# Kernel optimization log

Hardware: AMD Instinct MI355X
Metric: run time of the kernel (lower is better)

The kernel has to match this reference:

```python
import jax, jax.numpy as jnp
import numpy as np

N, IN, OUT = 8192, 4096, 4096
EPS = 1e-5


def setup_inputs() -> dict:
    key = jax.random.key(0)
    k1, k2, k3, k4, k5 = jax.random.split(key, 5)
    return {
        "input": jax.random.normal(k1, (N, IN), dtype=jnp.float32),
        "weight": jax.random.randint(k2, (OUT, IN // 8), 0, 256, dtype=jnp.int32),
        "weight_scale": jax.random.uniform(k3, (OUT,), dtype=jnp.float32, minval=0.5, maxval=1.5),
        "input_factor": jax.random.uniform(k4, (IN,), dtype=jnp.float32, minval=0.5, maxval=1.5),
        "bias": jax.random.normal(k5, (OUT,), dtype=jnp.float32) * 0.01,
    }


def _unpack_pm1(weight_packed, dtype):
    # weight_packed: [OUT, IN//8] packed bytes; bit b of byte j -> column j*8+b
    shifts = jnp.arange(8, dtype=weight_packed.dtype)  # [8]
    bits = (weight_packed[:, :, None] >> shifts) & 1   # [OUT, IN//8, 8]
    w = (1 - 2 * bits).astype(dtype)                   # bit 0 -> +1, bit 1 -> -1
    return w.reshape(weight_packed.shape[0], -1)        # [OUT, IN]


def reference(input, weight, weight_scale, input_factor, bias):
    x = input * input_factor[None, :]                   # [N, IN]
    w = _unpack_pm1(weight, x.dtype)                    # [OUT, IN]
    out = jnp.einsum("ni,oi->no", x, w)                # [N, OUT]
    out = out * weight_scale[None, :]
    # LayerNorm over OUT, no affine
    mean = jnp.mean(out, axis=-1, keepdims=True)
    var = jnp.var(out, axis=-1, keepdims=True)
    out = (out - mean) * jax.lax.rsqrt(var + EPS)
    return out + bias[None, :]
```

## Files before the change

### kernel.cpp

```cpp
#include <hip/hip_runtime.h>
#include <hip/hip_bf16.h>
#include <stdint.h>

#define N_ROWS 8192
#define IN_DIM 4096
#define OUT_DIM 4096
#define EPS 1e-5f
#define QSCALE 16.0f
#define INV_QS 0.0625f

typedef __attribute__((ext_vector_type(4))) int i32x4;
typedef __attribute__((ext_vector_type(16))) char c8x16;
typedef __attribute__((ext_vector_type(8))) char c8x8;

typedef const __attribute__((address_space(1))) void gbl_void_t;
typedef __attribute__((address_space(3))) void lds_void_t;

__device__ __forceinline__ void gload_lds16(const void* g, void* l) {
    __builtin_amdgcn_global_load_lds((gbl_void_t*)g, (lds_void_t*)l, 16, 0, 0);
}

__global__ __launch_bounds__(256) void scale_quant_kernel(
    const float* __restrict__ input, const float* __restrict__ factor,
    char* __restrict__ xq)
{
    long long idx = (long long)blockIdx.x * blockDim.x + threadIdx.x;
    long long base = idx * 16;
    if (base >= (long long)N_ROWS * IN_DIM) return;
    int col = (int)(base & (IN_DIM - 1));
    c8x16 r;
    #pragma unroll
    for (int q = 0; q < 4; ++q) {
        float4 a = *(const float4*)(input + base + q * 4);
        float4 f = *(const float4*)(factor + col + q * 4);
        float v[4] = {a.x*f.x, a.y*f.y, a.z*f.z, a.w*f.w};
        #pragma unroll
        for (int j = 0; j < 4; ++j) {
            int t = __float2int_rn(v[j] * QSCALE);
            t = t > 127 ? 127 : (t < -127 ? -127 : t);
            r[q * 4 + j] = (char)t;
        }
    }
    *(c8x16*)(xq + base) = r;
}

__global__ __launch_bounds__(256) void unpack_kernel(
    const int* __restrict__ wpacked, char* __restrict__ wq)
{
    int idx = blockIdx.x * blockDim.x + threadIdx.x;
    if (idx >= OUT_DIM * (IN_DIM / 8)) return;
    unsigned byte = (unsigned)wpacked[idx];
    c8x8 r;
    #pragma unroll
    for (int b = 0; b < 8; ++b)
        r[b] = (char)(1 - 2 * (int)((byte >> b) & 1u));
    *(c8x8*)(wq + (long long)idx * 8) = r;
}


template<int M0, int KS>
__device__ __forceinline__ void read_a4(i32x4 (&f)[4], const char* ap, int lane) {
    int rb = (lane & 15) << 7, g = lane >> 4, x = lane & 7;
    #pragma unroll
    for (int m = 0; m < 4; ++m)
        f[m] = *(const i32x4*)(ap + (M0 + m) * 2048 + rb + (((KS * 4 + g) ^ x) << 4));
}
template<int KS>
__device__ __forceinline__ void read_b4(i32x4 (&f)[4], const char* bp, int lane) {
    int rb = (lane & 15) << 7, g = lane >> 4, x = lane & 7;
    #pragma unroll
    for (int n = 0; n < 4; ++n)
        f[n] = *(const i32x4*)(bp + n * 2048 + rb + (((KS * 4 + g) ^ x) << 4));
}
template<int MQ>
__device__ __forceinline__ void mfma16(i32x4 (&acc)[8][4], i32x4 (&a4)[4], i32x4 (&b4)[4]) {
    #pragma unroll
    for (int i = 0; i < 4; ++i)
        #pragma unroll
        for (int j = 0; j < 4; ++j)
            acc[MQ * 4 + i][j] = __builtin_amdgcn_mfma_i32_16x16x64_i8(
                a4[i], b4[j], acc[MQ * 4 + i][j], 0, 0, 0);
}

__device__ __forceinline__ void stage_half(const char* g, char* l, int w) {
    gload_lds16(g + (size_t)(w * 16)     * IN_DIM, l + w * 2048);
    gload_lds16(g + (size_t)(w * 16 + 8) * IN_DIM, l + w * 2048 + 1024);
}

#define SYNC_PRE() do { __builtin_amdgcn_s_barrier(); \
    asm volatile("" ::: "memory"); \
    __builtin_amdgcn_s_setprio(1); } while(0)
#define SYNC_POST() do { __builtin_amdgcn_s_setprio(0); \
    asm volatile("" ::: "memory"); \
    __builtin_amdgcn_s_barrier(); } while(0)
#define VMCNT(n) asm volatile("s_waitcnt vmcnt(" #n ")" ::: "memory")

__global__ __launch_bounds__(512, 2) void gemm_kernel(
    const char* __restrict__ A, const char* __restrict__ B,
    const float* __restrict__ wscale, float* __restrict__ C)
{
    __shared__ char ldsb[131072];

    int nwg = gridDim.x;
    int bid = blockIdx.x;
    int swz = (bid & 7) * (nwg >> 3) + (bid >> 3);
    int bn = swz & 15;
    int bm = swz >> 4;
    int m0 = bm * 256, n0 = bn * 256;

    int tid = threadIdx.x;
    int lane = tid & 63;
    int w = tid >> 6;
    int wm = w >> 2, wn = w & 3, wh = wn >> 1;

    int srow = lane >> 3, sslot = (lane & 7) ^ srow;
    const char* Ag = A + (size_t)(m0 + srow) * IN_DIM + sslot * 16;
    const char* Bg = B + (size_t)(n0 + srow) * IN_DIM + sslot * 16;
    const size_t H = (size_t)128 * IN_DIM;

    char* L = ldsb;
    const char* ap0 = ldsb + wm * 16384;
    const char* ap1 = ap0 + 65536;
    const char* bp0 = ldsb + 32768 + wh * 16384 + (wn & 1) * 8192;
    const char* bp1 = bp0 + 65536;

    i32x4 afl[4], afh[4], bf0[4], bf1[4];
    i32x4 acc[8][4] = {};

    stage_half(Bg,           L + 32768,  w);
    stage_half(Bg + H,       L + 49152,  w);
    stage_half(Ag,           L + 0,      w);
    stage_half(Ag + H,       L + 16384,  w);
    stage_half(Bg + 128,     L + 98304,  w);
    stage_half(Bg + H + 128, L + 114688, w);
    stage_half(Ag + 128,     L + 65536,  w);
    VMCNT(6);
    __builtin_amdgcn_s_barrier();

    for (int it = 0; it < 15; ++it) {
        size_t s1 = (size_t)(2 * it + 1) * 128;
        size_t s2 = (size_t)(2 * it + 2) * 128;
        size_t s3 = (size_t)(2 * it + 3) * 128;

        read_a4<0, 0>(afl, ap0, lane);
        read_b4<0>(bf0, bp0, lane);
        if (wh == 0) read_b4<1>(bf1, bp0, lane);
        stage_half(Ag + H + s1, L + 81920, w);
        SYNC_PRE(); mfma16<0>(acc, afl, bf0); SYNC_POST();
        read_a4<4, 0>(afh, ap0, lane);
        if (wh == 1) read_b4<1>(bf1, bp0, lane);
        stage_half(Bg + s2, L + 32768, w);
        SYNC_PRE(); mfma16<1>(acc, afh, bf0); SYNC_POST();
        read_a4<0, 1>(afl, ap0, lane);
        if (wm == 0) read_a4<4, 1>(afh, ap0, lane);
        stage_half(Bg + H + s2, L + 49152, w);
        SYNC_PRE(); mfma16<0>(acc, afl, bf1); SYNC_POST();
        if (wm == 1) read_a4<4, 1>(afh, ap0, lane);
        stage_half(Ag + s2, L + 0, w);
        VMCNT(6);
        SYNC_PRE(); mfma16<1>(acc, afh, bf1); SYNC_POST();

        read_a4<0, 0>(afl, ap1, lane);
        read_b4<0>(bf0, bp1, lane);
        if (wh == 0) read_b4<1>(bf1, bp1, lane);
        stage_half(Ag + H + s2, L + 16384, w);
        SYNC_PRE(); mfma16<0>(acc, afl, bf0); SYNC_POST();
        read_a4<4, 0>(afh, ap1, lane);
        if (wh == 1) read_b4<1>(bf1, bp1, lane);
        stage_half(Bg + s3, L + 98304, w);
        SYNC_PRE(); mfma16<1>(acc, afh, bf0); SYNC_POST();
        read_a4<0, 1>(afl, ap1, lane);
        if (wm == 0) read_a4<4, 1>(afh, ap1, lane);
        stage_half(Bg + H + s3, L + 114688, w);
        SYNC_PRE(); mfma16<0>(acc, afl, bf1); SYNC_POST();
        if (wm == 1) read_a4<4, 1>(afh, ap1, lane);
        stage_half(Ag + s3, L + 65536, w);
        VMCNT(6);
        SYNC_PRE(); mfma16<1>(acc, afh, bf1); SYNC_POST();
    }

    {
        read_a4<0, 0>(afl, ap0, lane);
        read_b4<0>(bf0, bp0, lane);
        if (wh == 0) read_b4<1>(bf1, bp0, lane);
        stage_half(Ag + H + (size_t)31 * 128, L + 81920, w);
        SYNC_PRE(); mfma16<0>(acc, afl, bf0); SYNC_POST();
        read_a4<4, 0>(afh, ap0, lane);
        if (wh == 1) read_b4<1>(bf1, bp0, lane);
        SYNC_PRE(); mfma16<1>(acc, afh, bf0); SYNC_POST();
        read_a4<0, 1>(afl, ap0, lane);
        if (wm == 0) read_a4<4, 1>(afh, ap0, lane);
        SYNC_PRE(); mfma16<0>(acc, afl, bf1); SYNC_POST();
        if (wm == 1) read_a4<4, 1>(afh, ap0, lane);
        VMCNT(0);
        SYNC_PRE(); mfma16<1>(acc, afh, bf1); SYNC_POST();
        read_a4<0, 0>(afl, ap1, lane);
        read_b4<0>(bf0, bp1, lane);
        if (wh == 0) read_b4<1>(bf1, bp1, lane);
        SYNC_PRE(); mfma16<0>(acc, afl, bf0); SYNC_POST();
        read_a4<4, 0>(afh, ap1, lane);
        if (wh == 1) read_b4<1>(bf1, bp1, lane);
        SYNC_PRE(); mfma16<1>(acc, afh, bf0); SYNC_POST();
        read_a4<0, 1>(afl, ap1, lane);
        if (wm == 0) read_a4<4, 1>(afh, ap1, lane);
        SYNC_PRE(); mfma16<0>(acc, afl, bf1); SYNC_POST();
        if (wm == 1) read_a4<4, 1>(afh, ap1, lane);
        SYNC_PRE(); mfma16<1>(acc, afh, bf1);
        __builtin_amdgcn_s_setprio(0);
    }

    int crow = m0 + wm * 128;
    int ccol = n0 + wn * 64;
    #pragma unroll
    for (int n = 0; n < 4; ++n) {
        int col = ccol + n * 16 + (lane & 15);
        float ws = wscale[col] * INV_QS;
        #pragma unroll
        for (int m = 0; m < 8; ++m) {
            int row0 = crow + m * 16 + (lane >> 4) * 4;
            #pragma unroll
            for (int r = 0; r < 4; ++r)
                C[(size_t)(row0 + r) * OUT_DIM + col] = (float)acc[m][n][r] * ws;
        }
    }
}

__global__ __launch_bounds__(256) void ln_kernel(
    float* __restrict__ out, const float* __restrict__ bias)
{
    int row = blockIdx.x;
    int tid = threadIdx.x;
    float* p = out + (long long)row * OUT_DIM;

    float4 v[4];
    float sum = 0.f, sumsq = 0.f;
    #pragma unroll
    for (int q = 0; q < 4; ++q) {
        v[q] = *(const float4*)(p + (q * 256 + tid) * 4);
        sum   += v[q].x + v[q].y + v[q].z + v[q].w;
        sumsq += v[q].x*v[q].x + v[q].y*v[q].y + v[q].z*v[q].z + v[q].w*v[q].w;
    }
    #pragma unroll
    for (int off = 32; off > 0; off >>= 1) {
        sum   += __shfl_down(sum, off);
        sumsq += __shfl_down(sumsq, off);
    }
    __shared__ float ssum[4], ssq[4];
    if ((tid & 63) == 0) { ssum[tid >> 6] = sum; ssq[tid >> 6] = sumsq; }
    __syncthreads();
    sum   = ssum[0] + ssum[1] + ssum[2] + ssum[3];
    sumsq = ssq[0] + ssq[1] + ssq[2] + ssq[3];
    float mean = sum * (1.0f / OUT_DIM);
    float var  = sumsq * (1.0f / OUT_DIM) - mean * mean;
    float inv  = rsqrtf(var + EPS);

    #pragma unroll
    for (int q = 0; q < 4; ++q) {
        int c = (q * 256 + tid) * 4;
        float4 b = *(const float4*)(bias + c);
        float4 r;
        r.x = (v[q].x - mean) * inv + b.x;
        r.y = (v[q].y - mean) * inv + b.y;
        r.z = (v[q].z - mean) * inv + b.z;
        r.w = (v[q].w - mean) * inv + b.w;
        *(float4*)(p + c) = r;
    }
}

extern "C" void kernel_launch(void* const* d_in, const int* in_sizes, int n_in,
                              void* d_out, int out_size, void* d_ws, size_t ws_size,
                              hipStream_t stream) {
    const float* input   = (const float*)d_in[0];
    const int*   weight  = (const int*)d_in[1];
    const float* wscale  = (const float*)d_in[2];
    const float* factor  = (const float*)d_in[3];
    const float* bias    = (const float*)d_in[4];
    float* out = (float*)d_out;

    char* xq = (char*)d_ws;
    char* wq = (char*)d_ws + (size_t)N_ROWS * IN_DIM;

    {
        long long total = (long long)N_ROWS * IN_DIM / 16;
        int blocks = (int)((total + 255) / 256);
        scale_quant_kernel<<<blocks, 256, 0, stream>>>(input, factor, xq);
    }
    {
        int total = OUT_DIM * (IN_DIM / 8);
        unpack_kernel<<<(total + 255) / 256, 256, 0, stream>>>(weight, wq);
    }
    {
        int grid = (N_ROWS / 256) * (OUT_DIM / 256);
        gemm_kernel<<<grid, 512, 0, stream>>>(xq, wq, wscale, out);
    }
    ln_kernel<<<N_ROWS, 256, 0, stream>>>(out, bias);
}
```

Baseline: 207.2 us.

## Replace fine-grained interleaved GEMM pipeline with simple whole-tile double buffering

Replaces the hand-interleaved schedule, which had eight barrier pairs per K-step and issued staggered half-tile loads, with a simpler double-buffered loop. Each tile now issues the next tile's global-to-LDS loads, waits on vmcnt, takes one barrier, reads all fragments, runs 64 MFMAs and takes a closing barrier. The aim is fewer barriers and simpler scheduling. In exchange it gives up fine-grained overlap between LDS reads and MFMAs, needs more fragment registers live at once, and shortens the prefetch distance.

New measurement: 209.1 us. Within noise of the previous version (+0.9%).

```diff
diff --git a/kernel.cpp b/kernel.cpp
--- a/kernel.cpp
+++ b/kernel.cpp
@@ -8,6 +8,7 @@
 #define EPS 1e-5f
 #define QSCALE 16.0f
 #define INV_QS 0.0625f
+#define HSTR ((size_t)128 * IN_DIM)
 
 typedef __attribute__((ext_vector_type(4))) int i32x4;
 typedef __attribute__((ext_vector_type(16))) char c8x16;
@@ -87,13 +88,38 @@
     gload_lds16(g + (size_t)(w * 16 + 8) * IN_DIM, l + w * 2048 + 1024);
 }
 
-#define SYNC_PRE() do { __builtin_amdgcn_s_barrier(); \
-    asm volatile("" ::: "memory"); \
-    __builtin_amdgcn_s_setprio(1); } while(0)
-#define SYNC_POST() do { __builtin_amdgcn_s_setprio(0); \
-    asm volatile("" ::: "memory"); \
-    __builtin_amdgcn_s_barrier(); } while(0)
-#define VMCNT(n) asm volatile("s_waitcnt vmcnt(" #n ")" ::: "memory")
+template<bool DO_STAGE>
+__device__ __forceinline__ void do_tile(
+    i32x4 (&acc)[8][4], const char* ap, const char* bp, int lane,
+    const char* Ags, const char* Bgs, char* Lst, int w)
+{
+    if constexpr (DO_STAGE) {
+        stage_half(Bgs,        Lst + 32768, w);
+        stage_half(Bgs + HSTR, Lst + 49152, w);
+        stage_half(Ags,        Lst + 0,     w);
+        stage_half(Ags + HSTR, Lst + 16384, w);
+        asm volatile("s_waitcnt vmcnt(8)" ::: "memory");
+    } else {
+        asm volatile("s_waitcnt vmcnt(0)" ::: "memory");
+    }
+    __builtin_amdgcn_s_barrier();
+    asm volatile("" ::: "memory");
+    __builtin_amdgcn_s_setprio(1);
+    i32x4 a0[4], a1[4], b0[4], a2[4], a3[4], b1[4];
+    read_a4<0, 0>(a0, ap, lane);
+    read_a4<4, 0>(a1, ap, lane);
+    read_b4<0>(b0, bp, lane);
+    read_a4<0, 1>(a2, ap, lane);
+    read_a4<4, 1>(a3, ap, lane);
+    read_b4<1>(b1, bp, lane);
+    mfma16<0>(acc, a0, b0);
+    mfma16<1>(acc, a1, b0);
+    mfma16<0>(acc, a2, b1);
+    mfma16<1>(acc, a3, b1);
+    __builtin_amdgcn_s_setprio(0);
+    asm volatile("" ::: "memory");
+    __builtin_amdgcn_s_barrier();
+}
 
 __global__ __launch_bounds__(512, 2) void gemm_kernel(
     const char* __restrict__ A, const char* __restrict__ B,
@@ -116,7 +142,6 @@
     int srow = lane >> 3, sslot = (lane & 7) ^ srow;
     const char* Ag = A + (size_t)(m0 + srow) * IN_DIM + sslot * 16;
     const char* Bg = B + (size_t)(n0 + srow) * IN_DIM + sslot * 16;
-    const size_t H = (size_t)128 * IN_DIM;
 
     char* L = ldsb;
     const char* ap0 = ldsb + wm * 16384;
@@ -124,90 +149,23 @@
     const char* bp0 = ldsb + 32768 + wh * 16384 + (wn & 1) * 8192;
     const char* bp1 = bp0 + 65536;
 
-    i32x4 afl[4], afh[4], bf0[4], bf1[4];
     i32x4 acc[8][4] = {};
 
-    stage_half(Bg,           L + 32768,  w);
-    stage_half(Bg + H,       L + 49152,  w);
-    stage_half(Ag,           L + 0,      w);
-    stage_half(Ag + H,       L + 16384,  w);
-    stage_half(Bg + 128,     L + 98304,  w);
-    stage_half(Bg + H + 128, L + 114688, w);
-    stage_half(Ag + 128,     L + 65536,  w);
-    VMCNT(6);
-    __builtin_amdgcn_s_barrier();
+    stage_half(Bg,        L + 32768, w);
+    stage_half(Bg + HSTR, L + 49152, w);
+    stage_half(Ag,        L + 0,     w);
+    stage_half(Ag + HSTR, L + 16384, w);
 
     for (int it = 0; it < 15; ++it) {
-        size_t s1 = (size_t)(2 * it + 1) * 128;
-        size_t s2 = (size_t)(2 * it + 2) * 128;
-        size_t s3 = (size_t)(2 * it + 3) * 128;
-
-        read_a4<0, 0>(afl, ap0, lane);
-        read_b4<0>(bf0, bp0, lane);
-        if (wh == 0) read_b4<1>(bf1, bp0, lane);
-        stage_half(Ag + H + s1, L + 81920, w);
-        SYNC_PRE(); mfma16<0>(acc, afl, bf0); SYNC_POST();
-        read_a4<4, 0>(afh, ap0, lane);
-        if (wh == 1) read_b4<1>(bf1, bp0, lane);
-        stage_half(Bg + s2, L + 32768, w);
-        SYNC_PRE(); mfma16<1>(acc, afh, bf0); SYNC_POST();
-        read_a4<0, 1>(afl, ap0, lane);
-        if (wm == 0) read_a4<4, 1>(afh, ap0, lane);
-        stage_half(Bg + H + s2, L + 49152, w);
-        SYNC_PRE(); mfma16<0>(acc, afl, bf1); SYNC_POST();
-        if (wm == 1) read_a4<4, 1>(afh, ap0, lane);
-        stage_half(Ag + s2, L + 0, w);
-        VMCNT(6);
-        SYNC_PRE(); mfma16<1>(acc, afh, bf1); SYNC_POST();
-
-        read_a4<0, 0>(afl, ap1, lane);
-        read_b4<0>(bf0, bp1, lane);
-        if (wh == 0) read_b4<1>(bf1, bp1, lane);
-        stage_half(Ag + H + s2, L + 16384, w);
-        SYNC_PRE(); mfma16<0>(acc, afl, bf0); SYNC_POST();
-        read_a4<4, 0>(afh, ap1, lane);
-        if (wh == 1) read_b4<1>(bf1, bp1, lane);
-        stage_half(Bg + s3, L + 98304, w);
-        SYNC_PRE(); mfma16<1>(acc, afh, bf0); SYNC_POST();
-        read_a4<0, 1>(afl, ap1, lane);
-        if (wm == 0) read_a4<4, 1>(afh, ap1, lane);
-        stage_half(Bg + H + s3, L + 114688, w);
-        SYNC_PRE(); mfma16<0>(acc, afl, bf1); SYNC_POST();
-        if (wm == 1) read_a4<4, 1>(afh, ap1, lane);
-        stage_half(Ag + s3, L + 65536, w);
-        VMCNT(6);
-        SYNC_PRE(); mfma16<1>(acc, afh, bf1); SYNC_POST();
-    }
-
-    {
-        read_a4<0, 0>(afl, ap0, lane);
-        read_b4<0>(bf0, bp0, lane);
-        if (wh == 0) read_b4<1>(bf1, bp0, lane);
-        stage_half(Ag + H + (size_t)31 * 128, L + 81920, w);
-        SYNC_PRE(); mfma16<0>(acc, afl, bf0); SYNC_POST();
-        read_a4<4, 0>(afh, ap0, lane);
-        if (wh == 1) read_b4<1>(bf1, bp0, lane);
-        SYNC_PRE(); mfma16<1>(acc, afh, bf0); SYNC_POST();
-        read_a4<0, 1>(afl, ap0, lane);
-        if (wm == 0) read_a4<4, 1>(afh, ap0, lane);
-        SYNC_PRE(); mfma16<0>(acc, afl, bf1); SYNC_POST();
-        if (wm == 1) read_a4<4, 1>(afh, ap0, lane);
-        VMCNT(0);
-        SYNC_PRE(); mfma16<1>(acc, afh, bf1); SYNC_POST();
-        read_a4<0, 0>(afl, ap1, lane);
-        read_b4<0>(bf0, bp1, lane);
-        if (wh == 0) read_b4<1>(bf1, bp1, lane);
-        SYNC_PRE(); mfma16<0>(acc, afl, bf0); SYNC_POST();
-        read_a4<4, 0>(afh, ap1, lane);
-        if (wh == 1) read_b4<1>(bf1, bp1, lane);
-        SYNC_PRE(); mfma16<1>(acc, afh, bf0); SYNC_POST();
-        read_a4<0, 1>(afl, ap1, lane);
-        if (wm == 0) read_a4<4, 1>(afh, ap1, lane);
-        SYNC_PRE(); mfma16<0>(acc, afl, bf1); SYNC_POST();
-        if (wm == 1) read_a4<4, 1>(afh, ap1, lane);
-        SYNC_PRE(); mfma16<1>(acc, afh, bf1);
-        __builtin_amdgcn_s_setprio(0);
-    }
+        const char* A1g = Ag + (size_t)(2 * it + 1) * 128;
+        const char* B1g = Bg + (size_t)(2 * it + 1) * 128;
+        const char* A2g = Ag + (size_t)(2 * it + 2) * 128;
+        const char* B2g = Bg + (size_t)(2 * it + 2) * 128;
+        do_tile<true>(acc, ap0, bp0, lane, A1g, B1g, L + 65536, w);
+        do_tile<true>(acc, ap1, bp1, lane, A2g, B2g, L + 0,     w);
+    }
+    do_tile<true >(acc, ap0, bp0, lane, Ag + (size_t)31 * 128, Bg + (size_t)31 * 128, L + 65536, w);
+    do_tile<false>(acc, ap1, bp1, lane, Ag, Bg, L, w);
 
     int crow = m0 + wm * 128;
     int ccol = n0 + wn * 64;
```
